# Performance work log

Measured on AMD Instinct MI355X. Metric: run time of the kernel, lower is better.

Reference implementation:

```python
import jax, jax.numpy as jnp
import numpy as np

H = 8  # num_heads
C = 512  # embed_dims
L = 3  # num_layers
SCALE = (C // H) ** -0.5


def _ln(x, g, b, eps=1e-5):
    mu = jnp.mean(x, axis=-1, keepdims=True)
    var = jnp.mean((x - mu) ** 2, axis=-1, keepdims=True)
    return g * (x - mu) / jnp.sqrt(var + eps) + b


def setup_inputs() -> dict:
    key = jax.random.key(0)
    ks = jax.random.split(key, 12)
    B, Nq, Nk = 16, 64, 4096
    s = 0.02
    return dict(
        queries=jax.random.normal(ks[0], (B, Nq, C), jnp.float32),
        feat=jax.random.normal(ks[1], (B, Nk, C), jnp.float32),
        extra_token=jax.random.normal(ks[2], (B, 1, C), jnp.float32),
        Wq=jax.random.normal(ks[3], (L, C, C), jnp.float32) * s,
        bq=jnp.zeros((L, C), jnp.float32),
        Wk=jax.random.normal(ks[4], (L, C, C), jnp.float32) * s,
        bk=jnp.zeros((L, C), jnp.float32),
        Wv=jax.random.normal(ks[5], (L, C, C), jnp.float32) * s,
        bv=jnp.zeros((L, C), jnp.float32),
        Wo=jax.random.normal(ks[6], (L, C, C), jnp.float32) * s,
        bo=jnp.zeros((L, C), jnp.float32),
        W1=jax.random.normal(ks[7], (L, C, 4 * C), jnp.float32) * s,
        b1=jnp.zeros((L, 4 * C), jnp.float32),
        W2=jax.random.normal(ks[8], (L, 4 * C, C), jnp.float32) * s,
        b2=jnp.zeros((L, C), jnp.float32),
        g2=jnp.ones((L, C), jnp.float32),
        beta2=jnp.zeros((L, C), jnp.float32),
        g3=jnp.ones((L, C), jnp.float32),
        beta3=jnp.zeros((L, C), jnp.float32),
    )


def reference(queries, feat, extra_token, Wq, bq, Wk, bk, Wv, bv, Wo, bo,
              W1, b1, W2, b2, g2, beta2, g3, beta3):
    B, Nq, _ = queries.shape
    Nk = feat.shape[1]
    hd = C // H
    # extra gating token is NOT projected through q: raw reshape -> [B,H,1,hd]
    eq = extra_token.reshape(B, 1, H, hd).transpose(0, 2, 1, 3)
    x = queries
    outs, attns, affs = [], [], []
    for i in range(L):
        q = (x @ Wq[i] + bq[i]).reshape(B, Nq, H, hd).transpose(0, 2, 1, 3)
        k = (feat @ Wk[i] + bk[i]).reshape(B, Nk, H, hd).transpose(0, 2, 1, 3)
        v = (feat @ Wv[i] + bv[i]).reshape(B, Nk, H, hd).transpose(0, 2, 1, 3)
        attn = jnp.einsum('bhqd,bhkd->bhqk', q, k) * SCALE  # pre-softmax scores
        # affinity gate from extra token, averaged over heads -> [B,1,1,Nk]
        aff = jax.nn.sigmoid(jnp.mean(
            jnp.einsum('bhod,bhkd->bhok', eq, k) * SCALE, axis=1, keepdims=True))
        p = aff * jax.nn.softmax(attn, axis=-1)  # gated probabilities
        o = jnp.einsum('bhqk,bhkd->bqhd', p, v).reshape(B, Nq, C)
        o = o @ Wo[i] + bo[i]
        x = _ln(x + o, g2[i], beta2[i])
        ff = jax.nn.relu(x @ W1[i] + b1[i]) @ W2[i] + b2[i]
        x = _ln(x + ff, g3[i], beta3[i])
        outs.append(x)
        attns.append(attn.sum(axis=1) / H)  # head-averaged pre-softmax scores
        affs.append(aff)
    return (jnp.stack(outs), jnp.stack(attns), jnp.stack(affs))
```

## Files before the change

### kernel.cpp

```cpp
#include <hip/hip_runtime.h>


typedef unsigned short u16;
typedef __attribute__((ext_vector_type(8))) short short8;
typedef __attribute__((ext_vector_type(4))) short short4v;
typedef __attribute__((ext_vector_type(4))) float f32x4;

__device__ __forceinline__ float b2f(u16 u) {
    union { unsigned int i; float f; } v; v.i = ((unsigned int)u) << 16; return v.f;
}
__device__ __forceinline__ u16 f2b(float f) {
    unsigned int x = __float_as_uint(f);
    x += 0x7fffu + ((x >> 16) & 1u);
    return (u16)(x >> 16);
}

__device__ __forceinline__ float waveSum(float v) {
#pragma unroll
    for (int o = 32; o > 0; o >>= 1) v += __shfl_xor(v, o);
    return v;
}
__device__ __forceinline__ float waveMax(float v) {
#pragma unroll
    for (int o = 32; o > 0; o >>= 1) v = fmaxf(v, __shfl_xor(v, o));
    return v;
}

__device__ __forceinline__ void gl_lds16(const void* g, void* l) {
    __builtin_amdgcn_global_load_lds(
        (__attribute__((address_space(1))) void*)g,
        (__attribute__((address_space(3))) void*)l, 16, 0, 0);
}

template<bool BIAS_ROW, bool HAS_BIAS, bool AFFC>
__global__ __launch_bounds__(512, 1) void gemm256x256_k(
    const u16* __restrict__ A, const u16* __restrict__ Bt,
    const float* __restrict__ bias, u16* __restrict__ Cout,
    int lda, int ldb, int ldc, long sA2, long sB2, long sC2,
    const float* __restrict__ affc)
{
    __shared__ u16 As[2][256][64];
    __shared__ u16 Bs[2][256][64];
    const int t = threadIdx.x;
    const int lane = t & 63;
    const int wave = t >> 6;

    const int gx = gridDim.x, gy = gridDim.y;
    const int nwg = gx * gy * gridDim.z;
    int id;
    {
        const int orig = blockIdx.x + blockIdx.y * gx + blockIdx.z * gx * gy;
        const int qq = nwg >> 3, rr = nwg & 7;
        const int xcd = orig & 7, sub = orig >> 3;
        id = (xcd < rr ? xcd * (qq + 1) : rr * (qq + 1) + (xcd - rr) * qq) + sub;
    }
    const int bx = id % gx;
    const int by = (id / gx) % gy;
    const int z  = id / (gx * gy);

    A  += (long)z * sA2;
    Bt += (long)z * sB2;
    const long cbase = (long)z * sC2;
    const int n0 = bx * 256;
    const int m0 = by * 256;
    const int wm = wave >> 2;
    const int wn = wave & 3;
    const int rl = lane & 15, uq = lane >> 4;
    const int srow = lane >> 3;
    const int up   = lane & 7;

    f32x4 acc[8][4];
#pragma unroll
    for (int i = 0; i < 8; ++i)
#pragma unroll
        for (int j = 0; j < 4; ++j) acc[i][j] = (f32x4){0.f, 0.f, 0.f, 0.f};

    auto stage = [&](int buf, int kt) {
        const int k0 = kt * 64;
#pragma unroll
        for (int r = 0; r < 4; ++r) {
            const int row = r * 64 + wave * 8 + srow;
            const int ul = up ^ (row & 7);
            gl_lds16(A + (long)(m0 + row) * lda + k0 + ul * 8,
                     &As[buf][r * 64 + wave * 8][0]);
        }
#pragma unroll
        for (int r = 0; r < 4; ++r) {
            const int row = r * 64 + wave * 8 + srow;
            const int ul = up ^ (row & 7);
            gl_lds16(Bt + (long)(n0 + row) * ldb + k0 + ul * 8,
                     &Bs[buf][r * 64 + wave * 8][0]);
        }
    };

    auto compute = [&](int buf) {
#pragma unroll
        for (int kc = 0; kc < 2; ++kc) {
            short8 af[8], bf[4];
#pragma unroll
            for (int i = 0; i < 8; ++i) {
                const int R = wm * 128 + i * 16 + rl;
                af[i] = *(const short8*)(&As[buf][R][((kc * 4 + uq) ^ (R & 7)) * 8]);
            }
#pragma unroll
            for (int j = 0; j < 4; ++j) {
                const int R = wn * 64 + j * 16 + rl;
                bf[j] = *(const short8*)(&Bs[buf][R][((kc * 4 + uq) ^ (R & 7)) * 8]);
            }
            __builtin_amdgcn_s_setprio(1);
#pragma unroll
            for (int i = 0; i < 8; ++i)
#pragma unroll
                for (int j = 0; j < 4; ++j)
                    acc[i][j] = __builtin_amdgcn_mfma_f32_16x16x32_bf16(
                        af[i], bf[j], acc[i][j], 0, 0, 0);
            __builtin_amdgcn_s_setprio(0);
        }
    };

    stage(0, 0);
    __syncthreads();
    int buf = 0;
#pragma unroll
    for (int kt = 0; kt < 8; ++kt) {
        if (kt + 1 < 8) stage(buf ^ 1, kt + 1);
        compute(buf);
        __syncthreads();
        buf ^= 1;
    }

    const int r0 = (lane >> 4) * 4;
    const int c0 = lane & 15;
#pragma unroll
    for (int i = 0; i < 8; ++i) {
#pragma unroll
        for (int j = 0; j < 4; ++j) {
#pragma unroll
            for (int r = 0; r < 4; ++r) {
                const int row = m0 + wm * 128 + i * 16 + r0 + r;
                const int col = n0 + wn * 64 + j * 16 + c0;
                float v = acc[i][j][r];
                if constexpr (HAS_BIAS) {
                    if constexpr (BIAS_ROW) v += bias[row]; else v += bias[col];
                }
                if constexpr (AFFC) v *= affc[(long)z * 4096 + col];
                Cout[cbase + (long)row * ldc + col] = f2b(v);
            }
        }
    }
}

template<int TM, int TN, bool OUT_BF16, bool RELU, bool BIAS_ROW, bool HAS_BIAS,
         bool AFFC, bool SMAX>
__global__ __launch_bounds__(256) void gemm_bt_k(
    const u16* __restrict__ A, const u16* __restrict__ Bt,
    const float* __restrict__ bias, void* __restrict__ Cout,
    int K, int lda, int ldb, int ldc,
    int bdiv, long sA1, long sA2, long sB1, long sB2, long sC1, long sC2,
    float alpha, const float* __restrict__ affc, const float2* __restrict__ stats)
{
    __shared__ u16 As[TM][64];
    __shared__ u16 Bs[TN][64];
    const int t = threadIdx.x;
    const int lane = t & 63;
    const int wave = t >> 6;
    const int z = blockIdx.z;
    const int zq = z / bdiv, zr = z % bdiv;
    A  += (long)zq * sA1 + (long)zr * sA2;
    Bt += (long)zq * sB1 + (long)zr * sB2;
    const long cbase = (long)zq * sC1 + (long)zr * sC2;
    const int n0 = blockIdx.x * TN;
    const int m0 = blockIdx.y * TM;
    constexpr int FM = TM / 32, FN = TN / 32;
    const int wr = wave >> 1, wc = wave & 1;
    const int rl = lane & 15, uq = lane >> 4;

    float2 st[FM];
    if constexpr (SMAX) {
#pragma unroll
        for (int i = 0; i < FM; ++i)
            st[i] = stats[zr * 64 + m0 + wr * (TM / 2) + i * 16 + rl];
    }

    f32x4 acc[FM][FN];
#pragma unroll
    for (int i = 0; i < FM; ++i)
#pragma unroll
        for (int j = 0; j < FN; ++j) acc[i][j] = (f32x4){0.f, 0.f, 0.f, 0.f};

    const int srow = lane >> 3;
    const int up   = lane & 7;

    for (int k0 = 0; k0 < K; k0 += 64) {
        __syncthreads();
#pragma unroll
        for (int r = 0; r < TM / 32; ++r) {
            const int br = (wave * (TM / 32) + r) * 8;
            const int row = br + srow;
            const int ul = up ^ (row & 7);
            gl_lds16(A + (long)(m0 + row) * lda + k0 + ul * 8, &As[br][0]);
        }
#pragma unroll
        for (int r = 0; r < TN / 32; ++r) {
            const int br = (wave * (TN / 32) + r) * 8;
            const int row = br + srow;
            const int ul = up ^ (row & 7);
            gl_lds16(Bt + (long)(n0 + row) * ldb + k0 + ul * 8, &Bs[br][0]);
        }
        __syncthreads();

#pragma unroll
        for (int kc = 0; kc < 2; ++kc) {
            short8 af[FM], bf[FN];
#pragma unroll
            for (int i = 0; i < FM; ++i) {
                const int R = wr * (TM / 2) + i * 16 + rl;
                af[i] = *(const short8*)(&As[R][((kc * 4 + uq) ^ (R & 7)) * 8]);
                if constexpr (SMAX) {
#pragma unroll
                    for (int e = 0; e < 8; ++e)
                        af[i][e] = (short)f2b(
                            __expf(b2f((u16)af[i][e]) - st[i].x) * st[i].y);
                }
            }
#pragma unroll
            for (int j = 0; j < FN; ++j) {
                const int R = wc * (TN / 2) + j * 16 + rl;
                bf[j] = *(const short8*)(&Bs[R][((kc * 4 + uq) ^ (R & 7)) * 8]);
            }
#pragma unroll
            for (int i = 0; i < FM; ++i)
#pragma unroll
                for (int j = 0; j < FN; ++j)
                    acc[i][j] = __builtin_amdgcn_mfma_f32_16x16x32_bf16(
                        af[i], bf[j], acc[i][j], 0, 0, 0);
        }
    }

    const int r0 = (lane >> 4) * 4;
    const int c0 = lane & 15;
#pragma unroll
    for (int i = 0; i < FM; ++i) {
#pragma unroll
        for (int j = 0; j < FN; ++j) {
#pragma unroll
            for (int r = 0; r < 4; ++r) {
                const int row = m0 + wr * (TM / 2) + i * 16 + r0 + r;
                const int col = n0 + wc * (TN / 2) + j * 16 + c0;
                float v = acc[i][j][r] * alpha;
                if constexpr (HAS_BIAS) {
                    if constexpr (BIAS_ROW) v += bias[row]; else v += bias[col];
                }
                if constexpr (AFFC) v *= affc[(long)zq * 4096 + col];
                if constexpr (RELU) v = fmaxf(v, 0.f);
                const long idx = cbase + (long)row * ldc + col;
                if constexpr (OUT_BF16) ((u16*)Cout)[idx] = f2b(v);
                else                    ((float*)Cout)[idx] = v;
            }
        }
    }
}

__global__ __launch_bounds__(256) void smstats_k(
    const u16* __restrict__ S, float2* __restrict__ stats,
    float* __restrict__ attns)
{
    const int bq = blockIdx.x;
    const int b = bq >> 6, q = bq & 63;
    const int t = threadIdx.x;
    const int w = t >> 6, lane = t & 63;
    __shared__ float red[4];
    const int kb = t * 16;

    float attnacc[16];
#pragma unroll
    for (int j = 0; j < 16; ++j) attnacc[j] = 0.f;

    for (int h = 0; h < 8; ++h) {
        const long roff = (((long)(b * 8 + h)) * 64 + q) * 4096;
        const u16* Srow = S + roff;
        float v[16];
        short8 s0 = *(const short8*)(Srow + kb);
        short8 s1 = *(const short8*)(Srow + kb + 8);
#pragma unroll
        for (int j = 0; j < 8; ++j) { v[j] = b2f((u16)s0[j]); v[8 + j] = b2f((u16)s1[j]); }

        float m = -3.0e38f;
#pragma unroll
        for (int j = 0; j < 16; ++j) m = fmaxf(m, v[j]);
        m = waveMax(m);
        __syncthreads();
        if (lane == 0) red[w] = m;
        __syncthreads();
        m = fmaxf(fmaxf(red[0], red[1]), fmaxf(red[2], red[3]));

        float s = 0.f;
#pragma unroll
        for (int j = 0; j < 16; ++j) s += __expf(v[j] - m);
        s = waveSum(s);
        __syncthreads();
        if (lane == 0) red[w] = s;
        __syncthreads();
        s = red[0] + red[1] + red[2] + red[3];

        if (t == 0) stats[(b * 8 + h) * 64 + q] = make_float2(m, 1.f / s);
#pragma unroll
        for (int j = 0; j < 16; ++j) attnacc[j] += v[j];
    }
    float* arow = attns + (long)bq * 4096;
#pragma unroll
    for (int j = 0; j < 16; ++j) arow[kb + j] = attnacc[j] * 0.125f;
}

__global__ __launch_bounds__(256) void pv_reduce_k(
    const float* __restrict__ part, u16* __restrict__ o16)
{
    const int i = blockIdx.x * 256 + threadIdx.x;
    const int d4 = i & 15;
    const int q  = (i >> 4) & 63;
    const int bh = i >> 10;
    const float* p = part + (long)bh * 4096 + q * 64 + d4 * 4;
    float4 s = {0.f, 0.f, 0.f, 0.f};
#pragma unroll
    for (int sp = 0; sp < 8; ++sp) {
        const float4 v = *(const float4*)(p + (long)sp * 524288);
        s.x += v.x; s.y += v.y; s.z += v.z; s.w += v.w;
    }
    const int b = bh >> 3, h = bh & 7;
    u16* o = o16 + (long)b * 32768 + q * 512 + h * 64 + d4 * 4;
    short4v r;
    r[0] = (short)f2b(s.x); r[1] = (short)f2b(s.y);
    r[2] = (short)f2b(s.z); r[3] = (short)f2b(s.w);
    *(short4v*)o = r;
}

__global__ __launch_bounds__(256) void ffred_k(
    const float* __restrict__ part, const float* __restrict__ bias,
    float* __restrict__ out)
{
    const int i = (blockIdx.x * 256 + threadIdx.x) * 4;
    const int c = i & 511;
    float4 s = *(const float4*)(part + i);
#pragma unroll
    for (int sp = 1; sp < 4; ++sp) {
        const float4 v = *(const float4*)(part + (long)sp * 524288 + i);
        s.x += v.x; s.y += v.y; s.z += v.z; s.w += v.w;
    }
    s.x += bias[c]; s.y += bias[c + 1]; s.z += bias[c + 2]; s.w += bias[c + 3];
    *(float4*)(out + i) = s;
}

__global__ __launch_bounds__(256) void umat_k(
    const float* __restrict__ Wk, const float* __restrict__ extra,
    float* __restrict__ u)
{
    __shared__ float ex[16][512];
    const int l = blockIdx.x;
    const int t = threadIdx.x;
    for (int i = t; i < 16 * 512 / 4; i += 256)
        ((float4*)&ex[0][0])[i] = ((const float4*)extra)[i];
    __syncthreads();
    const int lane = t & 63, wave = t >> 6;
    const int row = blockIdx.y * 4 + wave;
    const float* wrow = Wk + ((size_t)l * 512 + row) * 512 + lane * 8;
    float w[8];
#pragma unroll
    for (int j = 0; j < 8; ++j) w[j] = wrow[j];
    float s[16];
#pragma unroll
    for (int b = 0; b < 16; ++b) {
        float x = 0.f;
#pragma unroll
        for (int j = 0; j < 8; ++j) x += w[j] * ex[b][lane * 8 + j];
        s[b] = waveSum(x);
    }
    if (lane < 16) u[((size_t)l * 16 + lane) * 512 + row] = s[lane];
}

__global__ __launch_bounds__(256) void cbk_k(
    const float* __restrict__ bk, const float* __restrict__ extra,
    float* __restrict__ cb)
{
    const int gw = blockIdx.x * 4 + (threadIdx.x >> 6);
    const int lane = threadIdx.x & 63;
    const int l = gw >> 4, b = gw & 15;
    float s = 0.f;
#pragma unroll
    for (int j = 0; j < 8; ++j)
        s += extra[b * 512 + lane * 8 + j] * bk[l * 512 + lane * 8 + j];
    s = waveSum(s);
    if (lane == 0) cb[gw] = s;
}

__global__ __launch_bounds__(256) void cvt16_aff_k(
    const float* __restrict__ feat, u16* __restrict__ dst,
    const float* __restrict__ u, const float* __restrict__ cb,
    float* __restrict__ affb, float* __restrict__ affs_out)
{
    const int t = blockIdx.x * 256 + threadIdx.x;
    const long i = (long)t * 8;
    const int lane = threadIdx.x & 63;
    const int r = t >> 6;
    const int b = r >> 12;
    const float4 a0 = *(const float4*)(feat + i);
    const float4 a1 = *(const float4*)(feat + i + 4);
    short8 o;
    o[0] = (short)f2b(a0.x); o[1] = (short)f2b(a0.y);
    o[2] = (short)f2b(a0.z); o[3] = (short)f2b(a0.w);
    o[4] = (short)f2b(a1.x); o[5] = (short)f2b(a1.y);
    o[6] = (short)f2b(a1.z); o[7] = (short)f2b(a1.w);
    *(short8*)(dst + i) = o;
    const float f[8] = {a0.x, a0.y, a0.z, a0.w, a1.x, a1.y, a1.z, a1.w};
#pragma unroll
    for (int l = 0; l < 3; ++l) {
        const float* ur = u + ((size_t)l * 16 + b) * 512 + lane * 8;
        float s = 0.f;
#pragma unroll
        for (int j = 0; j < 8; ++j) s += f[j] * ur[j];
        s = waveSum(s);
        if (lane == 0) {
            const float av = 1.f / (1.f + __expf(-0.015625f * (s + cb[l * 16 + b])));
            affb[l * 65536 + r] = av;
            affs_out[l * 65536 + r] = av;
        }
    }
}

template<bool WRITE_OUT>
__global__ __launch_bounds__(256) void ln_k(
    float* __restrict__ x, const float* __restrict__ add,
    const float* __restrict__ g, const float* __restrict__ be,
    u16* __restrict__ x16, float* __restrict__ outp)
{
    const int r = blockIdx.x, t = threadIdx.x;
    const int w = t >> 6, lane = t & 63;
    __shared__ float red[4];
    float* xr = x + (long)r * 512;
    const float* ar = add + (long)r * 512;
    const float v0 = xr[2 * t]     + ar[2 * t];
    const float v1 = xr[2 * t + 1] + ar[2 * t + 1];
    float s = waveSum(v0 + v1);
    if (lane == 0) red[w] = s;
    __syncthreads();
    s = red[0] + red[1] + red[2] + red[3];
    const float mu = s * (1.f / 512.f);
    const float d0 = v0 - mu, d1 = v1 - mu;
    __syncthreads();
    float vs = waveSum(d0 * d0 + d1 * d1);
    if (lane == 0) red[w] = vs;
    __syncthreads();
    vs = red[0] + red[1] + red[2] + red[3];
    const float rs = rsqrtf(vs * (1.f / 512.f) + 1e-5f);
    const float o0 = g[2 * t]     * d0 * rs + be[2 * t];
    const float o1 = g[2 * t + 1] * d1 * rs + be[2 * t + 1];
    xr[2 * t] = o0; xr[2 * t + 1] = o1;
    x16[(long)r * 512 + 2 * t]     = f2b(o0);
    x16[(long)r * 512 + 2 * t + 1] = f2b(o1);
    if constexpr (WRITE_OUT) {
        outp[(long)r * 512 + 2 * t]     = o0;
        outp[(long)r * 512 + 2 * t + 1] = o1;
    }
}

__global__ __launch_bounds__(256) void initx_k(
    const float* __restrict__ src, float* __restrict__ x, u16* __restrict__ x16)
{
    const long i = ((long)blockIdx.x * 256 + threadIdx.x) * 8;
    const float4 a = *(const float4*)(src + i);
    const float4 b = *(const float4*)(src + i + 4);
    *(float4*)(x + i) = a;
    *(float4*)(x + i + 4) = b;
    short8 r;
    r[0] = (short)f2b(a.x); r[1] = (short)f2b(a.y); r[2] = (short)f2b(a.z); r[3] = (short)f2b(a.w);
    r[4] = (short)f2b(b.x); r[5] = (short)f2b(b.y); r[6] = (short)f2b(b.z); r[7] = (short)f2b(b.w);
    *(short8*)(x16 + i) = r;
}

__global__ __launch_bounds__(256) void transpose_w_k(
    const float* __restrict__ W, u16* __restrict__ WT, int K, int N)
{
    __shared__ float tile[32][33];
    const int z = blockIdx.z;
    W  += (size_t)z * K * N;
    WT += (size_t)z * K * N;
    const int n0 = blockIdx.x * 32, k0 = blockIdx.y * 32;
    const int tx = threadIdx.x & 31, ty = threadIdx.x >> 5;
#pragma unroll
    for (int j = 0; j < 32; j += 8)
        tile[ty + j][tx] = W[(size_t)(k0 + ty + j) * N + n0 + tx];
    __syncthreads();
#pragma unroll
    for (int j = 0; j < 32; j += 8)
        WT[(size_t)(n0 + ty + j) * K + k0 + tx] = f2b(tile[tx][ty + j]);
}

extern "C" void kernel_launch(void* const* d_in, const int* in_sizes, int n_in,
                              void* d_out, int out_size, void* d_ws, size_t ws_size,
                              hipStream_t stream)
{
    (void)in_sizes; (void)n_in; (void)out_size; (void)ws_size;
    const float* queries = (const float*)d_in[0];
    const float* feat    = (const float*)d_in[1];
    const float* extra   = (const float*)d_in[2];
    const float* Wq = (const float*)d_in[3];  const float* bq = (const float*)d_in[4];
    const float* Wk = (const float*)d_in[5];  const float* bk = (const float*)d_in[6];
    const float* Wv = (const float*)d_in[7];  const float* bv = (const float*)d_in[8];
    const float* Wo = (const float*)d_in[9];  const float* bo = (const float*)d_in[10];
    const float* W1 = (const float*)d_in[11]; const float* b1 = (const float*)d_in[12];
    const float* W2 = (const float*)d_in[13]; const float* b2 = (const float*)d_in[14];
    const float* g2 = (const float*)d_in[15]; const float* be2 = (const float*)d_in[16];
    const float* g3 = (const float*)d_in[17]; const float* be3 = (const float*)d_in[18];

    char* wsb = (char*)d_ws;
    size_t off = 0;
    auto alloc = [&](size_t bytes) -> char* {
        char* p = wsb + off; off += (bytes + 255) & ~(size_t)255; return p;
    };
    u16*  feat16 = (u16*)alloc(33554432ull * 2);
    u16*  WqT = (u16*)alloc(786432ull * 2);
    u16*  WkT = (u16*)alloc(786432ull * 2);
    u16*  WvT = (u16*)alloc(786432ull * 2);
    u16*  WoT = (u16*)alloc(786432ull * 2);
    u16*  W1T = (u16*)alloc(3145728ull * 2);
    u16*  W2T = (u16*)alloc(3145728ull * 2);
    u16*  K16 = (u16*)alloc(33554432ull * 2);
    u16*  VT16 = (u16*)alloc(33554432ull * 2);
    u16*  q16 = (u16*)alloc(524288ull * 2);
    u16*  S16 = (u16*)alloc(33554432ull * 2);
    float* affb  = (float*)alloc(196608ull * 4);
    u16*  o16 = (u16*)alloc(524288ull * 2);
    float* oproj = (float*)alloc(524288ull * 4);
    float* xb    = (float*)alloc(524288ull * 4);
    u16*  x16 = (u16*)alloc(524288ull * 2);
    u16*  h116 = (u16*)alloc(2097152ull * 2);
    float* ffb   = (float*)alloc(524288ull * 4);
    float* uvec  = (float*)alloc(24576ull * 4);
    float* cb    = (float*)alloc(48ull * 4);
    float2* stats = (float2*)alloc(8192ull * 8);
    float* partPV = (float*)K16;
    float* part2  = (float*)VT16;

    float* out_f = (float*)d_out;
    float* outs_base  = out_f;
    float* attns_base = out_f + 1572864;
    float* affs_base  = out_f + 14155776;

    umat_k<<<dim3(3, 128), 256, 0, stream>>>(Wk, extra, uvec);
    cbk_k<<<12, 256, 0, stream>>>(bk, extra, cb);
    cvt16_aff_k<<<16384, 256, 0, stream>>>(feat, feat16, uvec, cb, affb, affs_base);
    initx_k<<<256, 256, 0, stream>>>(queries, xb, x16);
    transpose_w_k<<<dim3(16, 16, 3), 256, 0, stream>>>(Wq, WqT, 512, 512);
    transpose_w_k<<<dim3(16, 16, 3), 256, 0, stream>>>(Wk, WkT, 512, 512);
    transpose_w_k<<<dim3(16, 16, 3), 256, 0, stream>>>(Wv, WvT, 512, 512);
    transpose_w_k<<<dim3(16, 16, 3), 256, 0, stream>>>(Wo, WoT, 512, 512);
    transpose_w_k<<<dim3(64, 16, 3), 256, 0, stream>>>(W1, W1T, 512, 2048);
    transpose_w_k<<<dim3(16, 64, 3), 256, 0, stream>>>(W2, W2T, 2048, 512);

    for (int i = 0; i < 3; ++i) {
        gemm256x256_k<false, true, false><<<dim3(2, 256, 1), 512, 0, stream>>>(
            feat16, WkT + i * 262144, bk + i * 512, K16,
            512, 512, 512, 0, 0, 0, nullptr);
        gemm256x256_k<true, true, true><<<dim3(16, 2, 16), 512, 0, stream>>>(
            WvT + i * 262144, feat16, bv + i * 512, VT16,
            512, 512, 4096, 0, 2097152, 2097152, affb + i * 65536);
        gemm_bt_k<64, 64, true, false, false, true, false, false>
            <<<dim3(8, 16, 1), 256, 0, stream>>>(
            x16, WqT + i * 262144, bq + i * 512, q16,
            512, 512, 512, 512, 1, 0, 0, 0, 0, 0, 0, 1.f, nullptr, nullptr);
        gemm_bt_k<64, 128, true, false, false, false, false, false>
            <<<dim3(32, 1, 128), 256, 0, stream>>>(
            q16, K16, nullptr, S16,
            64, 512, 512, 4096, 8, 32768, 64, 2097152, 64, 2097152, 262144,
            0.125f, nullptr, nullptr);
        smstats_k<<<1024, 256, 0, stream>>>(
            S16, stats, attns_base + (size_t)i * 4194304);
        gemm_bt_k<64, 64, false, false, false, false, false, true>
            <<<dim3(1, 1, 1024), 256, 0, stream>>>(
            S16, VT16, nullptr, partPV,
            512, 4096, 4096, 64, 128, 512, 262144, 512, 262144, 524288, 4096,
            1.f, nullptr, stats);
        pv_reduce_k<<<512, 256, 0, stream>>>(partPV, o16);
        gemm_bt_k<64, 64, false, false, false, true, false, false>
            <<<dim3(8, 16, 1), 256, 0, stream>>>(
            o16, WoT + i * 262144, bo + i * 512, oproj,
            512, 512, 512, 512, 1, 0, 0, 0, 0, 0, 0, 1.f, nullptr, nullptr);
        ln_k<false><<<1024, 256, 0, stream>>>(xb, oproj, g2 + i * 512, be2 + i * 512, x16, nullptr);
        gemm_bt_k<64, 128, true, true, false, true, false, false>
            <<<dim3(16, 16, 1), 256, 0, stream>>>(
            x16, W1T + (size_t)i * 1048576, b1 + i * 2048, h116,
            512, 512, 512, 2048, 1, 0, 0, 0, 0, 0, 0, 1.f, nullptr, nullptr);
        gemm_bt_k<64, 64, false, false, false, false, false, false>
            <<<dim3(8, 16, 4), 256, 0, stream>>>(
            h116, W2T + (size_t)i * 1048576, nullptr, part2,
            512, 2048, 2048, 512, 1, 512, 0, 512, 0, 524288, 0,
            1.f, nullptr, nullptr);
        ffred_k<<<512, 256, 0, stream>>>(part2, b2 + i * 512, ffb);
        ln_k<true><<<1024, 256, 0, stream>>>(xb, ffb, g3 + i * 512, be3 + i * 512, x16,
                                             outs_base + (size_t)i * 524288);
    }
}
```

Baseline: 777.3 us.

## Replace materialized score/softmax/PV pipeline with split-K flash attention

Adds a flash-attention kernel that computes QK^T, an online softmax and PV on chip for four key splits per (batch, head), plus a merge kernel that combines the partial outputs using their running max and sum. The head-averaged score output is now produced directly by one GEMM with K=512 over all heads (scale 1/64), which replaces the bf16 score tensor and the stats kernel. The aim is to stop writing and reading the large per-head score matrix and to drop several launches. In exchange, QK^T is computed twice (once for the averaged scores, once inside attention), and the affinity gate still relies on being folded into V. Where V is rounded to bf16 after the gate is applied, the results may change slightly.

Result: faster. 670.1 us (-13.8%).

```diff
diff --git a/kernel.cpp b/kernel.cpp
--- a/kernel.cpp
+++ b/kernel.cpp
@@ -20,16 +20,196 @@
     for (int o = 32; o > 0; o >>= 1) v += __shfl_xor(v, o);
     return v;
 }
-__device__ __forceinline__ float waveMax(float v) {
-#pragma unroll
-    for (int o = 32; o > 0; o >>= 1) v = fmaxf(v, __shfl_xor(v, o));
-    return v;
-}
 
 __device__ __forceinline__ void gl_lds16(const void* g, void* l) {
     __builtin_amdgcn_global_load_lds(
         (__attribute__((address_space(1))) void*)g,
         (__attribute__((address_space(3))) void*)l, 16, 0, 0);
+}
+
+__global__ __launch_bounds__(256) void fattn_k(
+    const u16* __restrict__ q16, const u16* __restrict__ K16,
+    const u16* __restrict__ VT16, float* __restrict__ Op,
+    float2* __restrict__ ml)
+{
+    __shared__ u16 Qs[64][64];
+    __shared__ u16 Ks[128][64];
+    __shared__ u16 Vs[64][128];
+    __shared__ u16 Ps[64][128];
+    const int t = threadIdx.x;
+    const int lane = t & 63;
+    const int w = t >> 6;
+    const int bh = blockIdx.y;
+    const int split = blockIdx.x;
+    const int b = bh >> 3, h = bh & 7;
+    const int kbase = split * 1024;
+    const int rl = lane & 15, uq = lane >> 4;
+    const int r0 = (lane >> 4) * 4;
+    const int c0 = lane & 15;
+    const int srow8 = lane >> 3, up8 = lane & 7;
+    const int srow4 = lane >> 4, up16 = lane & 15;
+
+#pragma unroll
+    for (int rnd = 0; rnd < 2; ++rnd) {
+        const int row = rnd * 32 + w * 8 + srow8;
+        const int ul = up8 ^ (row & 7);
+        gl_lds16(q16 + ((long)(b * 64 + row)) * 512 + h * 64 + ul * 8,
+                 &Qs[rnd * 32 + w * 8][0]);
+    }
+
+    f32x4 O[4];
+#pragma unroll
+    for (int n = 0; n < 4; ++n) O[n] = (f32x4){0.f, 0.f, 0.f, 0.f};
+    float m_run[4] = {-3.0e38f, -3.0e38f, -3.0e38f, -3.0e38f};
+    float l_run[4] = {0.f, 0.f, 0.f, 0.f};
+
+    const int R = w * 16 + rl;
+
+    for (int tt = 0; tt < 8; ++tt) {
+        __syncthreads();
+#pragma unroll
+        for (int rnd = 0; rnd < 4; ++rnd) {
+            const int row = rnd * 32 + w * 8 + srow8;
+            const int ul = up8 ^ (row & 7);
+            gl_lds16(K16 + ((long)(b * 4096 + kbase + tt * 128 + row)) * 512
+                         + h * 64 + ul * 8,
+                     &Ks[rnd * 32 + w * 8][0]);
+        }
+#pragma unroll
+        for (int rnd = 0; rnd < 4; ++rnd) {
+            const int row = rnd * 16 + w * 4 + srow4;
+            const int ul = up16 ^ (row & 15);
+            gl_lds16(VT16 + (long)b * 2097152 + ((long)(h * 64 + row)) * 4096
+                         + kbase + tt * 128 + ul * 8,
+                     &Vs[rnd * 16 + w * 4][0]);
+        }
+        __syncthreads();
+
+        f32x4 s[8];
+        short8 af[2];
+#pragma unroll
+        for (int kc = 0; kc < 2; ++kc)
+            af[kc] = *(const short8*)(&Qs[R][((kc * 4 + uq) ^ (R & 7)) * 8]);
+#pragma unroll
+        for (int j = 0; j < 8; ++j) {
+            s[j] = (f32x4){0.f, 0.f, 0.f, 0.f};
+            const int Rb = j * 16 + rl;
+#pragma unroll
+            for (int kc = 0; kc < 2; ++kc) {
+                short8 bf = *(const short8*)(&Ks[Rb][((kc * 4 + uq) ^ (Rb & 7)) * 8]);
+                s[j] = __builtin_amdgcn_mfma_f32_16x16x32_bf16(af[kc], bf, s[j], 0, 0, 0);
+            }
+        }
+#pragma unroll
+        for (int j = 0; j < 8; ++j)
+#pragma unroll
+            for (int r = 0; r < 4; ++r) s[j][r] *= 0.125f;
+
+        float mv[4];
+#pragma unroll
+        for (int r = 0; r < 4; ++r) {
+            float m = s[0][r];
+#pragma unroll
+            for (int j = 1; j < 8; ++j) m = fmaxf(m, s[j][r]);
+#pragma unroll
+            for (int mask = 1; mask < 16; mask <<= 1)
+                m = fmaxf(m, __shfl_xor(m, mask));
+            mv[r] = m;
+        }
+        float al[4], rs[4];
+#pragma unroll
+        for (int r = 0; r < 4; ++r) {
+            const float mn = fmaxf(m_run[r], mv[r]);
+            al[r] = __expf(m_run[r] - mn);
+            m_run[r] = mn;
+            rs[r] = 0.f;
+        }
+#pragma unroll
+        for (int j = 0; j < 8; ++j)
+#pragma unroll
+            for (int r = 0; r < 4; ++r) {
+                s[j][r] = __expf(s[j][r] - m_run[r]);
+                rs[r] += s[j][r];
+            }
+#pragma unroll
+        for (int r = 0; r < 4; ++r) {
+#pragma unroll
+            for (int mask = 1; mask < 16; mask <<= 1)
+                rs[r] += __shfl_xor(rs[r], mask);
+            l_run[r] = l_run[r] * al[r] + rs[r];
+        }
+#pragma unroll
+        for (int n = 0; n < 4; ++n)
+#pragma unroll
+            for (int r = 0; r < 4; ++r) O[n][r] *= al[r];
+
+#pragma unroll
+        for (int j = 0; j < 8; ++j)
+#pragma unroll
+            for (int r = 0; r < 4; ++r) {
+                const int row = w * 16 + r0 + r;
+                const int col = j * 16 + c0;
+                Ps[row][(((col >> 3) ^ (row & 15)) << 3) + (col & 7)] = f2b(s[j][r]);
+            }
+#pragma unroll
+        for (int kc4 = 0; kc4 < 4; ++kc4) {
+            const short8 afp = *(const short8*)(&Ps[R][(((kc4 * 4 + uq) ^ (R & 15)) << 3)]);
+#pragma unroll
+            for (int n = 0; n < 4; ++n) {
+                const int Rv = n * 16 + rl;
+                const short8 bfv = *(const short8*)(&Vs[Rv][(((kc4 * 4 + uq) ^ (Rv & 15)) << 3)]);
+                O[n] = __builtin_amdgcn_mfma_f32_16x16x32_bf16(afp, bfv, O[n], 0, 0, 0);
+            }
+        }
+    }
+
+    const long obase = ((long)(split * 128 + bh)) * 64;
+#pragma unroll
+    for (int n = 0; n < 4; ++n)
+#pragma unroll
+        for (int r = 0; r < 4; ++r) {
+            const int q = w * 16 + r0 + r;
+            Op[(obase + q) * 64 + n * 16 + c0] = O[n][r];
+        }
+    if (c0 == 0) {
+#pragma unroll
+        for (int r = 0; r < 4; ++r) {
+            const int q = w * 16 + r0 + r;
+            ml[obase + q] = make_float2(m_run[r], l_run[r]);
+        }
+    }
+}
+
+__global__ __launch_bounds__(256) void fmerge_k(
+    const float* __restrict__ Op, const float2* __restrict__ ml,
+    u16* __restrict__ o16)
+{
+    const int i = blockIdx.x * 256 + threadIdx.x;
+    const int d4 = i & 15;
+    const int q  = (i >> 4) & 63;
+    const int bh = i >> 10;
+    const float2 m0 = ml[((long)(0 * 128 + bh)) * 64 + q];
+    const float2 m1 = ml[((long)(1 * 128 + bh)) * 64 + q];
+    const float2 m2 = ml[((long)(2 * 128 + bh)) * 64 + q];
+    const float2 m3 = ml[((long)(3 * 128 + bh)) * 64 + q];
+    const float m = fmaxf(fmaxf(m0.x, m1.x), fmaxf(m2.x, m3.x));
+    const float e0 = __expf(m0.x - m), e1 = __expf(m1.x - m);
+    const float e2 = __expf(m2.x - m), e3 = __expf(m3.x - m);
+    const float inv = 1.f / (m0.y * e0 + m1.y * e1 + m2.y * e2 + m3.y * e3);
+    const float4 v0 = *(const float4*)(Op + (((long)(0 * 128 + bh)) * 64 + q) * 64 + d4 * 4);
+    const float4 v1 = *(const float4*)(Op + (((long)(1 * 128 + bh)) * 64 + q) * 64 + d4 * 4);
+    const float4 v2 = *(const float4*)(Op + (((long)(2 * 128 + bh)) * 64 + q) * 64 + d4 * 4);
+    const float4 v3 = *(const float4*)(Op + (((long)(3 * 128 + bh)) * 64 + q) * 64 + d4 * 4);
+    float4 acc;
+    acc.x = (v0.x * e0 + v1.x * e1 + v2.x * e2 + v3.x * e3) * inv;
+    acc.y = (v0.y * e0 + v1.y * e1 + v2.y * e2 + v3.y * e3) * inv;
+    acc.z = (v0.z * e0 + v1.z * e1 + v2.z * e2 + v3.z * e3) * inv;
+    acc.w = (v0.w * e0 + v1.w * e1 + v2.w * e2 + v3.w * e3) * inv;
+    const int b = bh >> 3, h = bh & 7;
+    short4v r;
+    r[0] = (short)f2b(acc.x); r[1] = (short)f2b(acc.y);
+    r[2] = (short)f2b(acc.z); r[3] = (short)f2b(acc.w);
+    *(short4v*)(o16 + (long)b * 32768 + q * 512 + h * 64 + d4 * 4) = r;
 }
 
 template<bool BIAS_ROW, bool HAS_BIAS, bool AFFC>
@@ -150,14 +330,12 @@
     }
 }
 
-template<int TM, int TN, bool OUT_BF16, bool RELU, bool BIAS_ROW, bool HAS_BIAS,
-         bool AFFC, bool SMAX>
+template<int TM, int TN, bool OUT_BF16, bool RELU, bool BIAS_ROW, bool HAS_BIAS>
 __global__ __launch_bounds__(256) void gemm_bt_k(
     const u16* __restrict__ A, const u16* __restrict__ Bt,
     const float* __restrict__ bias, void* __restrict__ Cout,
     int K, int lda, int ldb, int ldc,
-    int bdiv, long sA1, long sA2, long sB1, long sB2, long sC1, long sC2,
-    float alpha, const float* __restrict__ affc, const float2* __restrict__ stats)
+    long sA1, long sB1, long sC1, float alpha)
 {
     __shared__ u16 As[TM][64];
     __shared__ u16 Bs[TN][64];
@@ -165,23 +343,15 @@
     const int lane = t & 63;
     const int wave = t >> 6;
     const int z = blockIdx.z;
-    const int zq = z / bdiv, zr = z % bdiv;
-    A  += (long)zq * sA1 + (long)zr * sA2;
-    Bt += (long)zq * sB1 + (long)zr * sB2;
-    const long cbase = (long)zq * sC1 + (long)zr * sC2;
+    A  += (long)z * sA1;
+    Bt += (long)z * sB1;
+    const long cbase = (long)z * sC1;
     const int n0 = blockIdx.x * TN;
     const int m0 = blockIdx.y * TM;
     constexpr int FM = TM / 32, FN = TN / 32;
     const int wr = wave >> 1, wc = wave & 1;
     const int rl = lane & 15, uq = lane >> 4;
 
-    float2 st[FM];
-    if constexpr (SMAX) {
-#pragma unroll
-        for (int i = 0; i < FM; ++i)
-            st[i] = stats[zr * 64 + m0 + wr * (TM / 2) + i * 16 + rl];
-    }
-
     f32x4 acc[FM][FN];
 #pragma unroll
     for (int i = 0; i < FM; ++i)
@@ -216,12 +386,6 @@
             for (int i = 0; i < FM; ++i) {
                 const int R = wr * (TM / 2) + i * 16 + rl;
                 af[i] = *(const short8*)(&As[R][((kc * 4 + uq) ^ (R & 7)) * 8]);
-                if constexpr (SMAX) {
-#pragma unroll
-                    for (int e = 0; e < 8; ++e)
-                        af[i][e] = (short)f2b(
-                            __expf(b2f((u16)af[i][e]) - st[i].x) * st[i].y);
-                }
             }
 #pragma unroll
             for (int j = 0; j < FN; ++j) {
@@ -251,7 +415,6 @@
                 if constexpr (HAS_BIAS) {
                     if constexpr (BIAS_ROW) v += bias[row]; else v += bias[col];
                 }
-                if constexpr (AFFC) v *= affc[(long)zq * 4096 + col];
                 if constexpr (RELU) v = fmaxf(v, 0.f);
                 const long idx = cbase + (long)row * ldc + col;
                 if constexpr (OUT_BF16) ((u16*)Cout)[idx] = f2b(v);
@@ -259,79 +422,6 @@
             }
         }
     }
-}
-
-__global__ __launch_bounds__(256) void smstats_k(
-    const u16* __restrict__ S, float2* __restrict__ stats,
-    float* __restrict__ attns)
-{
-    const int bq = blockIdx.x;
-    const int b = bq >> 6, q = bq & 63;
-    const int t = threadIdx.x;
-    const int w = t >> 6, lane = t & 63;
-    __shared__ float red[4];
-    const int kb = t * 16;
-
-    float attnacc[16];
-#pragma unroll
-    for (int j = 0; j < 16; ++j) attnacc[j] = 0.f;
-
-    for (int h = 0; h < 8; ++h) {
-        const long roff = (((long)(b * 8 + h)) * 64 + q) * 4096;
-        const u16* Srow = S + roff;
-        float v[16];
-        short8 s0 = *(const short8*)(Srow + kb);
-        short8 s1 = *(const short8*)(Srow + kb + 8);
-#pragma unroll
-        for (int j = 0; j < 8; ++j) { v[j] = b2f((u16)s0[j]); v[8 + j] = b2f((u16)s1[j]); }
-
-        float m = -3.0e38f;
-#pragma unroll
-        for (int j = 0; j < 16; ++j) m = fmaxf(m, v[j]);
-        m = waveMax(m);
-        __syncthreads();
-        if (lane == 0) red[w] = m;
-        __syncthreads();
-        m = fmaxf(fmaxf(red[0], red[1]), fmaxf(red[2], red[3]));
-
-        float s = 0.f;
-#pragma unroll
-        for (int j = 0; j < 16; ++j) s += __expf(v[j] - m);
-        s = waveSum(s);
-        __syncthreads();
-        if (lane == 0) red[w] = s;
-        __syncthreads();
-        s = red[0] + red[1] + red[2] + red[3];
-
-        if (t == 0) stats[(b * 8 + h) * 64 + q] = make_float2(m, 1.f / s);
-#pragma unroll
-        for (int j = 0; j < 16; ++j) attnacc[j] += v[j];
-    }
-    float* arow = attns + (long)bq * 4096;
-#pragma unroll
-    for (int j = 0; j < 16; ++j) arow[kb + j] = attnacc[j] * 0.125f;
-}
-
-__global__ __launch_bounds__(256) void pv_reduce_k(
-    const float* __restrict__ part, u16* __restrict__ o16)
-{
-    const int i = blockIdx.x * 256 + threadIdx.x;
-    const int d4 = i & 15;
-    const int q  = (i >> 4) & 63;
-    const int bh = i >> 10;
-    const float* p = part + (long)bh * 4096 + q * 64 + d4 * 4;
-    float4 s = {0.f, 0.f, 0.f, 0.f};
-#pragma unroll
-    for (int sp = 0; sp < 8; ++sp) {
-        const float4 v = *(const float4*)(p + (long)sp * 524288);
-        s.x += v.x; s.y += v.y; s.z += v.z; s.w += v.w;
-    }
-    const int b = bh >> 3, h = bh & 7;
-    u16* o = o16 + (long)b * 32768 + q * 512 + h * 64 + d4 * 4;
-    short4v r;
-    r[0] = (short)f2b(s.x); r[1] = (short)f2b(s.y);
-    r[2] = (short)f2b(s.z); r[3] = (short)f2b(s.w);
-    *(short4v*)o = r;
 }
 
 __global__ __launch_bounds__(256) void ffred_k(
@@ -526,7 +616,8 @@
     u16*  K16 = (u16*)alloc(33554432ull * 2);
     u16*  VT16 = (u16*)alloc(33554432ull * 2);
     u16*  q16 = (u16*)alloc(524288ull * 2);
-    u16*  S16 = (u16*)alloc(33554432ull * 2);
+    float* Op  = (float*)alloc(4194304ull * 4);
+    float2* ml = (float2*)alloc(32768ull * 8);
     float* affb  = (float*)alloc(196608ull * 4);
     u16*  o16 = (u16*)alloc(524288ull * 2);
     float* oproj = (float*)alloc(524288ull * 4);
@@ -536,9 +627,7 @@
     float* ffb   = (float*)alloc(524288ull * 4);
     float* uvec  = (float*)alloc(24576ull * 4);
     float* cb    = (float*)alloc(48ull * 4);
-    float2* stats = (float2*)alloc(8192ull * 8);
-    float* partPV = (float*)K16;
-    float* part2  = (float*)VT16;
+    float* part2 = (float*)VT16;
 
     float* out_f = (float*)d_out;
     float* outs_base  = out_f;
@@ -563,37 +652,29 @@
         gemm256x256_k<true, true, true><<<dim3(16, 2, 16), 512, 0, stream>>>(
             WvT + i * 262144, feat16, bv + i * 512, VT16,
             512, 512, 4096, 0, 2097152, 2097152, affb + i * 65536);
-        gemm_bt_k<64, 64, true, false, false, true, false, false>
+        gemm_bt_k<64, 64, true, false, false, true>
             <<<dim3(8, 16, 1), 256, 0, stream>>>(
             x16, WqT + i * 262144, bq + i * 512, q16,
-            512, 512, 512, 512, 1, 0, 0, 0, 0, 0, 0, 1.f, nullptr, nullptr);
-        gemm_bt_k<64, 128, true, false, false, false, false, false>
-            <<<dim3(32, 1, 128), 256, 0, stream>>>(
-            q16, K16, nullptr, S16,
-            64, 512, 512, 4096, 8, 32768, 64, 2097152, 64, 2097152, 262144,
-            0.125f, nullptr, nullptr);
-        smstats_k<<<1024, 256, 0, stream>>>(
-            S16, stats, attns_base + (size_t)i * 4194304);
-        gemm_bt_k<64, 64, false, false, false, false, false, true>
-            <<<dim3(1, 1, 1024), 256, 0, stream>>>(
-            S16, VT16, nullptr, partPV,
-            512, 4096, 4096, 64, 128, 512, 262144, 512, 262144, 524288, 4096,
-            1.f, nullptr, stats);
-        pv_reduce_k<<<512, 256, 0, stream>>>(partPV, o16);
-        gemm_bt_k<64, 64, false, false, false, true, false, false>
+            512, 512, 512, 512, 0, 0, 0, 1.f);
+        gemm_bt_k<64, 128, false, false, false, false>
+            <<<dim3(32, 1, 16), 256, 0, stream>>>(
+            q16, K16, nullptr, attns_base + (size_t)i * 4194304,
+            512, 512, 512, 4096, 32768, 2097152, 262144, 0.015625f);
+        fattn_k<<<dim3(4, 128), 256, 0, stream>>>(q16, K16, VT16, Op, ml);
+        fmerge_k<<<512, 256, 0, stream>>>(Op, ml, o16);
+        gemm_bt_k<64, 64, false, false, false, true>
             <<<dim3(8, 16, 1), 256, 0, stream>>>(
             o16, WoT + i * 262144, bo + i * 512, oproj,
-            512, 512, 512, 512, 1, 0, 0, 0, 0, 0, 0, 1.f, nullptr, nullptr);
+            512, 512, 512, 512, 0, 0, 0, 1.f);
         ln_k<false><<<1024, 256, 0, stream>>>(xb, oproj, g2 + i * 512, be2 + i * 512, x16, nullptr);
-        gemm_bt_k<64, 128, true, true, false, true, false, false>
+        gemm_bt_k<64, 128, true, true, false, true>
             <<<dim3(16, 16, 1), 256, 0, stream>>>(
             x16, W1T + (size_t)i * 1048576, b1 + i * 2048, h116,
-            512, 512, 512, 2048, 1, 0, 0, 0, 0, 0, 0, 1.f, nullptr, nullptr);
-        gemm_bt_k<64, 64, false, false, false, false, false, false>
+            512, 512, 512, 2048, 0, 0, 0, 1.f);
+        gemm_bt_k<64, 64, false, false, false, false>
             <<<dim3(8, 16, 4), 256, 0, stream>>>(
             h116, W2T + (size_t)i * 1048576, nullptr, part2,
-            512, 2048, 2048, 512, 1, 512, 0, 512, 0, 524288, 0,
-            1.f, nullptr, nullptr);
+            512, 2048, 2048, 512, 512, 512, 524288, 1.f);
         ffred_k<<<512, 256, 0, stream>>>(part2, b2 + i * 512, ffb);
         ln_k<true><<<1024, 256, 0, stream>>>(xb, ffb, g3 + i * 512, be3 + i * 512, x16,
                                              outs_base + (size_t)i * 524288);
```
